# Performance work log

Hardware: AMD Instinct MI355X
Metric: run time of the kernel (lower is better)

Reference implementation:

```python
import jax, jax.numpy as jnp
import numpy as np


def _hungarian(a):
    """Jonker-Volgenant / Kuhn-Munkres shortest-augmenting-path LAP solver.
    a: (n, n) float numpy cost matrix. Returns col_ind (int64, len n) such that
    row i is matched to column col_ind[i] (row_ind is implicitly arange(n),
    exactly like scipy.optimize.linear_sum_assignment on a square matrix).
    """
    n = a.shape[0]
    INF = np.inf
    u = np.zeros(n + 1)
    v = np.zeros(n + 1)
    p = np.zeros(n + 1, dtype=np.int64)   # p[j] = row currently matched to column j
    way = np.zeros(n + 1, dtype=np.int64)
    for i in range(1, n + 1):
        p[0] = i
        j0 = 0
        minv = np.full(n + 1, INF)
        used = np.zeros(n + 1, dtype=bool)
        while True:
            used[j0] = True
            i0 = p[j0]
            cur = a[i0 - 1] - u[i0] - v[1:]          # reduced costs of row i0
            free = ~used[1:]
            better = free & (cur < minv[1:])
            minv[1:] = np.where(better, cur, minv[1:])
            way[1:] = np.where(better, j0, way[1:])
            cand = np.where(free, minv[1:], INF)
            j1 = int(np.argmin(cand)) + 1
            delta = cand[j1 - 1]
            u[p[used]] += delta
            v[used] -= delta
            minv[1:] = np.where(free, minv[1:] - delta, minv[1:])
            j0 = j1
            if p[j0] == 0:
                break
        while j0 != 0:                               # augment along alternating path
            j1 = int(way[j0])
            p[j0] = p[j1]
            j0 = j1
    col_ind = np.zeros(n, dtype=np.int64)
    col_ind[p[1:] - 1] = np.arange(n)
    return col_ind


def _matching(input, target):
    sx = jnp.sum(input * input, axis=-1)
    sy = jnp.sum(target * target, axis=-1)
    cost = sx[:, :, None] + sy[:, None, :] - 2.0 * jnp.einsum('bkd,bmd->bkm', input, target)
    cost_np = np.asarray(jax.device_get(cost), dtype=np.float64)
    perms = np.stack([_hungarian(c) for c in cost_np])  # (B, k)
    return jnp.asarray(perms)


def setup_inputs() -> dict:
    key = jax.random.key(0)
    k1, k2 = jax.random.split(key)
    B, K, D = 512, 128, 512
    return {
        "input": jax.random.normal(k1, (B, K, D), dtype=jnp.float32),
        "target": jax.random.normal(k2, (B, K, D), dtype=jnp.float32),
    }


def reference(input, target):
    # Hungarian assignment is computed on detached costs (constant wrt grads).
    perms = _matching(input, target)                       # (B, k)
    matched_target = jnp.take_along_axis(target, perms[:, :, None], axis=1)
    # Per-batch mean over (k, d), then mean over batch == global mean (equal sizes).
    return jnp.mean((input - matched_target) ** 2)
```

## Files before the change

kernel.cpp:

```cpp
#include <hip/hip_runtime.h>
#include <hip/hip_bf16.h>

#define K_PTS 128
#define DIM   512
#define BK    32
#define XS_STRIDE 132

__device__ __forceinline__ int rdlane_i(int v, int lane) {
    return __builtin_amdgcn_readlane(v, lane);
}
__device__ __forceinline__ float rdlane_f(float v, int lane) {
    return __int_as_float(__builtin_amdgcn_readlane(__float_as_int(v), lane));
}
__device__ __forceinline__ void wave_fence() {
    asm volatile("s_waitcnt lgkmcnt(0)" ::: "memory");
}

#define DPP_ID 0xFFFFFFFFu

template <int CTRL, int RM>
__device__ __forceinline__ unsigned dpp_min1(unsigned k) {
    unsigned o = (unsigned)__builtin_amdgcn_update_dpp((int)DPP_ID, (int)k, CTRL, RM, 0xF, false);
    return min(k, o);
}
__device__ __forceinline__ unsigned wave_min_u32(unsigned k) {
    k = dpp_min1<0x111, 0xF>(k);
    k = dpp_min1<0x112, 0xF>(k);
    k = dpp_min1<0x114, 0xF>(k);
    k = dpp_min1<0x118, 0xF>(k);
    k = dpp_min1<0x142, 0xA>(k);
    k = dpp_min1<0x143, 0xC>(k);
    return (unsigned)rdlane_i((int)k, 63);
}
template <int CTRL, int RM>
__device__ __forceinline__ void dpp_min2(unsigned& best, unsigned& sec) {
    unsigned ob = (unsigned)__builtin_amdgcn_update_dpp((int)DPP_ID, (int)best, CTRL, RM, 0xF, false);
    unsigned os = (unsigned)__builtin_amdgcn_update_dpp((int)DPP_ID, (int)sec,  CTRL, RM, 0xF, false);
    sec  = min(max(best, ob), min(sec, os));
    best = min(best, ob);
}
__device__ __forceinline__ void wave_min2_u32(unsigned& best, unsigned& sec) {
    dpp_min2<0x111, 0xF>(best, sec);
    dpp_min2<0x112, 0xF>(best, sec);
    dpp_min2<0x114, 0xF>(best, sec);
    dpp_min2<0x118, 0xF>(best, sec);
    dpp_min2<0x142, 0xA>(best, sec);
    dpp_min2<0x143, 0xC>(best, sec);
    best = (unsigned)rdlane_i((int)best, 63);
    sec  = (unsigned)rdlane_i((int)sec, 63);
}

__global__ __launch_bounds__(256, 2)
void hungarian_mse_kernel(const float* __restrict__ X, const float* __restrict__ Y,
                          float* __restrict__ out, float inv_total) {
    const int b = blockIdx.x;
    const int t = threadIdx.x;

    __shared__ float A[K_PTS * K_PTS];
    __shared__ float sx_sh[K_PTS];
    __shared__ float sy_sh[K_PTS];
    __shared__ float u_sh[K_PTS];
    __shared__ int   rmatch[K_PTS];
    __shared__ int   wl[512];
    __shared__ int   wl_n;

    float* Xs = A;
    float* Ys = A + BK * XS_STRIDE;

    const float* Xg = X + (size_t)b * K_PTS * DIM;
    const float* Yg = Y + (size_t)b * K_PTS * DIM;

    float acc[8][8];
#pragma unroll
    for (int i = 0; i < 8; ++i)
#pragma unroll
        for (int j = 0; j < 8; ++j) acc[i][j] = 0.0f;

    float nrm = 0.0f;
    const int tx = t & 15;
    const int ty = t >> 4;

    for (int k0 = 0; k0 < DIM; k0 += BK) {
        __syncthreads();
#pragma unroll
        for (int i = 0; i < 4; ++i) {
            int idx = t + i * 256;
            int r  = idx >> 3;
            int kq = idx & 7;
            float4 vx = *(const float4*)(Xg + r * DIM + k0 + kq * 4);
            float4 vy = *(const float4*)(Yg + r * DIM + k0 + kq * 4);
            int kb = kq * 4;
            Xs[(kb + 0) * XS_STRIDE + r] = vx.x;
            Xs[(kb + 1) * XS_STRIDE + r] = vx.y;
            Xs[(kb + 2) * XS_STRIDE + r] = vx.z;
            Xs[(kb + 3) * XS_STRIDE + r] = vx.w;
            Ys[(kb + 0) * XS_STRIDE + r] = vy.x;
            Ys[(kb + 1) * XS_STRIDE + r] = vy.y;
            Ys[(kb + 2) * XS_STRIDE + r] = vy.z;
            Ys[(kb + 3) * XS_STRIDE + r] = vy.w;
        }
        __syncthreads();
        for (int kk = 0; kk < BK; ++kk) {
            const float* xrow = Xs + kk * XS_STRIDE;
            const float* yrow = Ys + kk * XS_STRIDE;
            float4 xa = *(const float4*)(xrow + ty * 8);
            float4 xb = *(const float4*)(xrow + ty * 8 + 4);
            float4 ya = *(const float4*)(yrow + tx * 8);
            float4 yb = *(const float4*)(yrow + tx * 8 + 4);
            float av[8] = {xa.x, xa.y, xa.z, xa.w, xb.x, xb.y, xb.z, xb.w};
            float bv[8] = {ya.x, ya.y, ya.z, ya.w, yb.x, yb.y, yb.z, yb.w};
#pragma unroll
            for (int i = 0; i < 8; ++i)
#pragma unroll
                for (int j = 0; j < 8; ++j)
                    acc[i][j] = fmaf(av[i], bv[j], acc[i][j]);
        }
        if (t < 128) {
#pragma unroll
            for (int kk = 0; kk < BK; ++kk) {
                float v = Xs[kk * XS_STRIDE + t];
                nrm = fmaf(v, v, nrm);
            }
        } else {
#pragma unroll
            for (int kk = 0; kk < BK; ++kk) {
                float v = Ys[kk * XS_STRIDE + (t - 128)];
                nrm = fmaf(v, v, nrm);
            }
        }
    }
    if (t < 128) sx_sh[t] = nrm; else sy_sh[t - 128] = nrm;
    if (t < 128) u_sh[t] = 0.0f;
    __syncthreads();
#pragma unroll
    for (int i = 0; i < 8; ++i) {
        int r = ty * 8 + i;
        float sxr = sx_sh[r];
        float4 o0, o1;
        o0.x = sxr + sy_sh[tx * 8 + 0] - 2.0f * acc[i][0];
        o0.y = sxr + sy_sh[tx * 8 + 1] - 2.0f * acc[i][1];
        o0.z = sxr + sy_sh[tx * 8 + 2] - 2.0f * acc[i][2];
        o0.w = sxr + sy_sh[tx * 8 + 3] - 2.0f * acc[i][3];
        o1.x = sxr + sy_sh[tx * 8 + 4] - 2.0f * acc[i][4];
        o1.y = sxr + sy_sh[tx * 8 + 5] - 2.0f * acc[i][5];
        o1.z = sxr + sy_sh[tx * 8 + 6] - 2.0f * acc[i][6];
        o1.w = sxr + sy_sh[tx * 8 + 7] - 2.0f * acc[i][7];
        *(float4*)&A[r * K_PTS + tx * 8]     = o0;
        *(float4*)&A[r * K_PTS + tx * 8 + 4] = o1;
    }
    __syncthreads();

    if (t < 64) {
        asm volatile("s_setprio 3");
        const int c0 = 2 * t, c1 = 2 * t + 1;
        float v0, v1;
        int p_lo = -1, p_hi = -1;

        rmatch[t] = -1; rmatch[t + 64] = -1;
        wave_fence();
        {
            float m0 = 1e30f, m1 = 1e30f;
            int a0 = 0, a1 = 0;
#pragma unroll 4
            for (int i = 0; i < K_PTS; ++i) {
                float2 cc = *(const float2*)&A[i * K_PTS + c0];
                if (cc.x < m0) { m0 = cc.x; a0 = i; }
                if (cc.y < m1) { m1 = cc.y; a1 = i; }
            }
            v0 = m0; v1 = m1;
            int w0 = atomicCAS(&rmatch[a0], -1, c0);
            if (w0 == -1) p_lo = a0;
            int w1 = atomicCAS(&rmatch[a1], -1, c1);
            if (w1 == -1) p_hi = a1;
        }
        wave_fence();

        *(float2*)&sy_sh[c0] = make_float2(v0, v1);
        wave_fence();
#pragma unroll
        for (int which = 0; which < 2; ++which) {
            int i  = t + which * 64;
            int j1 = rmatch[i];
            float mu = 1e30f;
            if (j1 >= 0) {
#pragma unroll 4
                for (int s = 0; s < 64; ++s) {
                    int jj = (s + t) & 63;
                    float2 cc = *(const float2*)&A[i * K_PTS + 2 * jj];
                    float2 vv = *(const float2*)&sy_sh[2 * jj];
                    float r0 = cc.x - vv.x;
                    float r1 = cc.y - vv.y;
                    if (2 * jj     != j1) mu = fminf(mu, r0);
                    if (2 * jj + 1 != j1) mu = fminf(mu, r1);
                }
            }
            sx_sh[i] = mu;
        }
        wave_fence();
        if (p_lo >= 0) { float mu = sx_sh[p_lo]; v0 = A[p_lo * K_PTS + c0] - mu; u_sh[p_lo] = mu; }
        if (p_hi >= 0) { float mu = sx_sh[p_hi]; v1 = A[p_hi * K_PTS + c1] - mu; u_sh[p_hi] = mu; }
        wave_fence();

        if (t == 0) {
            int n = 0;
            for (int i = 0; i < K_PTS; ++i) if (rmatch[i] < 0) wl[n++] = i;
            wl_n = n;
        }
        wave_fence();

        {
            int head = 0, tail = wl_n, steps = 0;
            while (head < tail && steps < 320) {
                ++steps;
                int i = wl[head++];
                float2 cc = *(const float2*)&A[i * K_PTS + c0];
                float r0 = fmaxf(cc.x - v0, 0.0f);
                float r1 = fmaxf(cc.y - v1, 0.0f);
                unsigned k0 = (__float_as_uint(r0) & 0xFFFFFF80u) | (unsigned)c0;
                unsigned k1 = (__float_as_uint(r1) & 0xFFFFFF80u) | (unsigned)c1;
                unsigned best = min(k0, k1), sec = max(k0, k1);
                wave_min2_u32(best, sec);
                int j1 = (int)(best & 127u);
                int j2 = (int)(sec & 127u);
                float mu = __uint_as_float(best & 0xFFFFFF80u);
                float nu = __uint_as_float(sec  & 0xFFFFFF80u);
                if (t == 0) u_sh[i] = nu;
                int kO = rdlane_i((j1 & 1) ? p_hi : p_lo, j1 >> 1);
                bool strict = (mu < nu);
                if (strict && t == (j1 >> 1)) {
                    float d = nu - mu;
                    if (j1 & 1) v1 -= d; else v0 -= d;
                }
                int jA = j1;
                if (!strict && kO >= 0) {
                    int k2 = rdlane_i((j2 & 1) ? p_hi : p_lo, j2 >> 1);
                    if (k2 < 0) jA = j2;
                }
                int kOld = rdlane_i((jA & 1) ? p_hi : p_lo, jA >> 1);
                if (t == (jA >> 1)) { if (jA & 1) p_hi = i; else p_lo = i; }
                if (t == 0) {
                    rmatch[i] = jA;
                    if (kOld >= 0) { rmatch[kOld] = -1; wl[tail] = kOld; }
                }
                if (kOld >= 0) ++tail;
                wave_fence();
            }
        }

        if (t == 0) {
            int n = 0;
            for (int i = 0; i < K_PTS; ++i) if (rmatch[i] < 0) wl[n++] = i;
            wl_n = n;
        }
        wave_fence();
        const int nfree = wl_n;

        for (int idx = 0; idx < nfree; ++idx) {
            int row = wl[idx];
            float u_lo_reg = u_sh[t];
            float u_hi_reg = u_sh[t + 64];
            float u_row = rdlane_f((row >= 64) ? u_hi_reg : u_lo_reg, row & 63);
            float2 rc = *(const float2*)&A[row * K_PTS + c0];
            float dist0 = fmaxf(rc.x - u_row - v0, 0.0f);
            float dist1 = fmaxf(rc.y - u_row - v1, 0.0f);
            int way0 = 128, way1 = 128;
            bool sc0 = false, sc1 = false;
            int j1 = 0;
            float D = 0.0f;

            while (true) {
                unsigned k0 = sc0 ? 0xFFFFFFFFu
                                  : ((__float_as_uint(dist0) & 0xFFFFFF80u) | (unsigned)c0);
                unsigned k1 = sc1 ? 0xFFFFFFFFu
                                  : ((__float_as_uint(dist1) & 0xFFFFFF80u) | (unsigned)c1);
                unsigned k = wave_min_u32(min(k0, k1));
                j1 = (int)(k & 127u);
                D  = __uint_as_float(k & 0xFFFFFF80u);
                int i1 = rdlane_i((j1 & 1) ? p_hi : p_lo, j1 >> 1);
                if (i1 < 0) break;

                if (j1 == c0) sc0 = true;
                if (j1 == c1) sc1 = true;

                float u_i1 = rdlane_f((i1 >= 64) ? u_hi_reg : u_lo_reg, i1 & 63);
                float2 aa = *(const float2*)&A[i1 * K_PTS + c0];
                float base = D - u_i1;
                if (!sc0) {
                    float cv = fmaxf((aa.x - v0) + base, 0.0f);
                    if (cv < dist0) { dist0 = cv; way0 = j1; }
                }
                if (!sc1) {
                    float cv = fmaxf((aa.y - v1) + base, 0.0f);
                    if (cv < dist1) { dist1 = cv; way1 = j1; }
                }
            }

            if (sc0) { float del = D - dist0; v0 -= del; u_sh[p_lo] += del; }
            if (sc1) { float del = D - dist1; v1 -= del; u_sh[p_hi] += del; }
            if (t == 0) u_sh[row] += D;

            int j0 = j1;
            while (true) {
                int lane0 = j0 >> 1;
                bool odd = (j0 & 1) != 0;
                int jp = rdlane_i(odd ? way1 : way0, lane0);
                int pv;
                if (jp == 128) pv = row;
                else           pv = rdlane_i((jp & 1) ? p_hi : p_lo, jp >> 1);
                if (!odd && lane0 == t) p_lo = pv;
                if ( odd && lane0 == t) p_hi = pv;
                if (jp == 128) break;
                j0 = jp;
            }
            wave_fence();
        }

        float tsum = A[p_lo * K_PTS + c0] + A[p_hi * K_PTS + c1];
#pragma unroll
        for (int m = 1; m <= 32; m <<= 1)
            tsum += __shfl_xor(tsum, m, 64);
        if (t == 0) atomicAdd(out, tsum * inv_total);
    }
}

extern "C" void kernel_launch(void* const* d_in, const int* in_sizes, int n_in,
                              void* d_out, int out_size, void* d_ws, size_t ws_size,
                              hipStream_t stream) {
    const float* X = (const float*)d_in[0];
    const float* Y = (const float*)d_in[1];
    float* out = (float*)d_out;

    const int total = in_sizes[0];
    const int B = total / (K_PTS * DIM);
    const float inv_total = 1.0f / (float)total;

    hipMemsetAsync(out, 0, out_size * sizeof(float), stream);
    hungarian_mse_kernel<<<dim3(B), dim3(256), 0, stream>>>(X, Y, out, inv_total);
}
```

Baseline: 683.2 us.

## Scan up to four tied-minimum columns per Dijkstra step in LAP search

```diff
diff --git a/kernel.cpp b/kernel.cpp
--- a/kernel.cpp
+++ b/kernel.cpp
@@ -273,25 +273,60 @@
                                   : ((__float_as_uint(dist0) & 0xFFFFFF80u) | (unsigned)c0);
                 unsigned k1 = sc1 ? 0xFFFFFFFFu
                                   : ((__float_as_uint(dist1) & 0xFFFFFF80u) | (unsigned)c1);
-                unsigned k = wave_min_u32(min(k0, k1));
-                j1 = (int)(k & 127u);
-                D  = __uint_as_float(k & 0xFFFFFF80u);
-                int i1 = rdlane_i((j1 & 1) ? p_hi : p_lo, j1 >> 1);
-                if (i1 < 0) break;
-
-                if (j1 == c0) sc0 = true;
-                if (j1 == c1) sc1 = true;
-
-                float u_i1 = rdlane_f((i1 >= 64) ? u_hi_reg : u_lo_reg, i1 & 63);
-                float2 aa = *(const float2*)&A[i1 * K_PTS + c0];
-                float base = D - u_i1;
-                if (!sc0) {
-                    float cv = fmaxf((aa.x - v0) + base, 0.0f);
-                    if (cv < dist0) { dist0 = cv; way0 = j1; }
-                }
-                if (!sc1) {
-                    float cv = fmaxf((aa.y - v1) + base, 0.0f);
-                    if (cv < dist1) { dist1 = cv; way1 = j1; }
+                unsigned kmin = wave_min_u32(min(k0, k1));
+                unsigned Dbits = kmin & 0xFFFFFF80u;
+                D = __uint_as_float(Dbits);
+
+                bool cand0 = !sc0 && ((k0 & 0xFFFFFF80u) == Dbits);
+                bool cand1 = !sc1 && ((k1 & 0xFFFFFF80u) == Dbits);
+
+                bool f0 = cand0 && (p_lo < 0);
+                bool f1 = cand1 && (p_hi < 0);
+                unsigned long long bfree = __ballot(f0 || f1);
+                if (bfree) {
+                    int l = __ffsll(bfree) - 1;
+                    unsigned long long bf0 = __ballot(f0);
+                    j1 = ((bf0 >> l) & 1ull) ? 2 * l : 2 * l + 1;
+                    break;
+                }
+
+                unsigned long long b0 = __ballot(cand0);
+                unsigned long long b1 = __ballot(cand1);
+                int colS[4], rowS[4];
+#pragma unroll
+                for (int s = 0; s < 4; ++s) {
+                    int col = -1;
+                    if (b0) { int l = __ffsll(b0) - 1; b0 &= b0 - 1; col = 2 * l; }
+                    else if (b1) { int l = __ffsll(b1) - 1; b1 &= b1 - 1; col = 2 * l + 1; }
+                    colS[s] = col;
+                    rowS[s] = (col >= 0) ? rdlane_i((col & 1) ? p_hi : p_lo, col >> 1) : -1;
+                }
+
+#pragma unroll
+                for (int s = 0; s < 4; ++s) {
+                    if (colS[s] == c0) sc0 = true;
+                    if (colS[s] == c1) sc1 = true;
+                }
+
+                float2 aaS[4];
+#pragma unroll
+                for (int s = 0; s < 4; ++s)
+                    if (colS[s] >= 0) aaS[s] = *(const float2*)&A[rowS[s] * K_PTS + c0];
+
+#pragma unroll
+                for (int s = 0; s < 4; ++s) {
+                    if (colS[s] >= 0) {
+                        float u_i = rdlane_f((rowS[s] >= 64) ? u_hi_reg : u_lo_reg, rowS[s] & 63);
+                        float base = D - u_i;
+                        if (!sc0) {
+                            float cv = fmaxf((aaS[s].x - v0) + base, 0.0f);
+                            if (cv < dist0) { dist0 = cv; way0 = colS[s]; }
+                        }
+                        if (!sc1) {
+                            float cv = fmaxf((aaS[s].y - v1) + base, 0.0f);
+                            if (cv < dist1) { dist1 = cv; way1 = colS[s]; }
+                        }
+                    }
                 }
             }
 
```

Measured after the change: 846.6 us. 23.9% more time.

## Cache per-lane cost columns in VGPRs for the Hungarian solver wave

Applied to the files above, without the earlier changes.

```diff
diff --git a/kernel.cpp b/kernel.cpp
--- a/kernel.cpp
+++ b/kernel.cpp
@@ -5,6 +5,9 @@
 #define DIM   512
 #define BK    32
 #define XS_STRIDE 132
+#define B_CAP 320
+
+typedef float f32x32 __attribute__((ext_vector_type(32)));
 
 __device__ __forceinline__ int rdlane_i(int v, int lane) {
     return __builtin_amdgcn_readlane(v, lane);
@@ -50,7 +53,7 @@
     sec  = (unsigned)rdlane_i((int)sec, 63);
 }
 
-__global__ __launch_bounds__(256, 2)
+__global__ __launch_bounds__(256, 1)
 void hungarian_mse_kernel(const float* __restrict__ X, const float* __restrict__ Y,
                           float* __restrict__ out, float inv_total) {
     const int b = blockIdx.x;
@@ -153,6 +156,40 @@
     if (t < 64) {
         asm volatile("s_setprio 3");
         const int c0 = 2 * t, c1 = 2 * t + 1;
+
+        f32x32 aL0, aL1, aL2, aL3;
+        f32x32 aH0, aH1, aH2, aH3;
+#pragma unroll
+        for (int r = 0; r < 32; ++r) {
+            float2 cc = *(const float2*)&A[r * K_PTS + c0];
+            aL0[r] = cc.x; aH0[r] = cc.y;
+        }
+#pragma unroll
+        for (int r = 0; r < 32; ++r) {
+            float2 cc = *(const float2*)&A[(r + 32) * K_PTS + c0];
+            aL1[r] = cc.x; aH1[r] = cc.y;
+        }
+#pragma unroll
+        for (int r = 0; r < 32; ++r) {
+            float2 cc = *(const float2*)&A[(r + 64) * K_PTS + c0];
+            aL2[r] = cc.x; aH2[r] = cc.y;
+        }
+#pragma unroll
+        for (int r = 0; r < 32; ++r) {
+            float2 cc = *(const float2*)&A[(r + 96) * K_PTS + c0];
+            aL3[r] = cc.x; aH3[r] = cc.y;
+        }
+
+        auto GETROW = [&](int i) -> float2 {
+            int q = i >> 5, m = i & 31;
+            float x, y;
+            if (q == 0)      { x = aL0[m]; y = aH0[m]; }
+            else if (q == 1) { x = aL1[m]; y = aH1[m]; }
+            else if (q == 2) { x = aL2[m]; y = aH2[m]; }
+            else             { x = aL3[m]; y = aH3[m]; }
+            return make_float2(x, y);
+        };
+
         float v0, v1;
         int p_lo = -1, p_hi = -1;
 
@@ -161,11 +198,25 @@
         {
             float m0 = 1e30f, m1 = 1e30f;
             int a0 = 0, a1 = 0;
-#pragma unroll 4
-            for (int i = 0; i < K_PTS; ++i) {
-                float2 cc = *(const float2*)&A[i * K_PTS + c0];
-                if (cc.x < m0) { m0 = cc.x; a0 = i; }
-                if (cc.y < m1) { m1 = cc.y; a1 = i; }
+#pragma unroll
+            for (int i = 0; i < 32; ++i) {
+                if (aL0[i] < m0) { m0 = aL0[i]; a0 = i; }
+                if (aH0[i] < m1) { m1 = aH0[i]; a1 = i; }
+            }
+#pragma unroll
+            for (int i = 0; i < 32; ++i) {
+                if (aL1[i] < m0) { m0 = aL1[i]; a0 = i + 32; }
+                if (aH1[i] < m1) { m1 = aH1[i]; a1 = i + 32; }
+            }
+#pragma unroll
+            for (int i = 0; i < 32; ++i) {
+                if (aL2[i] < m0) { m0 = aL2[i]; a0 = i + 64; }
+                if (aH2[i] < m1) { m1 = aH2[i]; a1 = i + 64; }
+            }
+#pragma unroll
+            for (int i = 0; i < 32; ++i) {
+                if (aL3[i] < m0) { m0 = aL3[i]; a0 = i + 96; }
+                if (aH3[i] < m1) { m1 = aH3[i]; a1 = i + 96; }
             }
             v0 = m0; v1 = m1;
             int w0 = atomicCAS(&rmatch[a0], -1, c0);
@@ -197,8 +248,8 @@
             sx_sh[i] = mu;
         }
         wave_fence();
-        if (p_lo >= 0) { float mu = sx_sh[p_lo]; v0 = A[p_lo * K_PTS + c0] - mu; u_sh[p_lo] = mu; }
-        if (p_hi >= 0) { float mu = sx_sh[p_hi]; v1 = A[p_hi * K_PTS + c1] - mu; u_sh[p_hi] = mu; }
+        if (p_lo >= 0) { float mu = sx_sh[p_lo]; v0 = GETROW(p_lo).x - mu; u_sh[p_lo] = mu; }
+        if (p_hi >= 0) { float mu = sx_sh[p_hi]; v1 = GETROW(p_hi).y - mu; u_sh[p_hi] = mu; }
         wave_fence();
 
         if (t == 0) {
@@ -210,10 +261,11 @@
 
         {
             int head = 0, tail = wl_n, steps = 0;
-            while (head < tail && steps < 320) {
+            while (head < tail && steps < B_CAP) {
                 ++steps;
-                int i = wl[head++];
-                float2 cc = *(const float2*)&A[i * K_PTS + c0];
+                int i = __builtin_amdgcn_readfirstlane(wl[head++]);
+                wave_fence();
+                float2 cc = GETROW(i);
                 float r0 = fmaxf(cc.x - v0, 0.0f);
                 float r1 = fmaxf(cc.y - v1, 0.0f);
                 unsigned k0 = (__float_as_uint(r0) & 0xFFFFFF80u) | (unsigned)c0;
@@ -256,11 +308,11 @@
         const int nfree = wl_n;
 
         for (int idx = 0; idx < nfree; ++idx) {
-            int row = wl[idx];
+            int row = __builtin_amdgcn_readfirstlane(wl[idx]);
             float u_lo_reg = u_sh[t];
             float u_hi_reg = u_sh[t + 64];
-            float u_row = rdlane_f((row >= 64) ? u_hi_reg : u_lo_reg, row & 63);
-            float2 rc = *(const float2*)&A[row * K_PTS + c0];
+            float u_row = u_sh[row];
+            float2 rc = GETROW(row);
             float dist0 = fmaxf(rc.x - u_row - v0, 0.0f);
             float dist1 = fmaxf(rc.y - u_row - v1, 0.0f);
             int way0 = 128, way1 = 128;
@@ -283,7 +335,7 @@
                 if (j1 == c1) sc1 = true;
 
                 float u_i1 = rdlane_f((i1 >= 64) ? u_hi_reg : u_lo_reg, i1 & 63);
-                float2 aa = *(const float2*)&A[i1 * K_PTS + c0];
+                float2 aa = GETROW(i1);
                 float base = D - u_i1;
                 if (!sc0) {
                     float cv = fmaxf((aa.x - v0) + base, 0.0f);
```

Result: slower. 834.5 us (+22.1%).

## Split cost GEMM and LAP solve into separate kernels with register-resident cost rows

Applied to the files above, without the earlier changes.

```diff
diff --git a/kernel.cpp b/kernel.cpp
--- a/kernel.cpp
+++ b/kernel.cpp
@@ -5,6 +5,7 @@
 #define DIM   512
 #define BK    32
 #define XS_STRIDE 132
+#define B_CAP 320
 
 __device__ __forceinline__ int rdlane_i(int v, int lane) {
     return __builtin_amdgcn_readlane(v, lane);
@@ -50,25 +51,31 @@
     sec  = (unsigned)rdlane_i((int)sec, 63);
 }
 
+#define GR1(k)  case (k): gr = arr[(k)]; break;
+#define GR4(k)  GR1(k) GR1((k)+1) GR1((k)+2) GR1((k)+3)
+#define GR16(k) GR4(k) GR4((k)+4) GR4((k)+8) GR4((k)+12)
+#define GR64(k) GR16(k) GR16((k)+16) GR16((k)+32) GR16((k)+48)
+#define GETROW(dst, idx) do { float2 gr;                      \
+    switch (idx) { GR64(0) GR64(64)                           \
+        default: gr = make_float2(0.0f, 0.0f); break; }       \
+    (dst) = gr; } while (0)
+
 __global__ __launch_bounds__(256, 2)
-void hungarian_mse_kernel(const float* __restrict__ X, const float* __restrict__ Y,
-                          float* __restrict__ out, float inv_total) {
+void cost_kernel(const float* __restrict__ X, const float* __restrict__ Y,
+                 float* __restrict__ G) {
     const int b = blockIdx.x;
     const int t = threadIdx.x;
 
-    __shared__ float A[K_PTS * K_PTS];
+    __shared__ float stage[2 * BK * XS_STRIDE];
     __shared__ float sx_sh[K_PTS];
     __shared__ float sy_sh[K_PTS];
-    __shared__ float u_sh[K_PTS];
-    __shared__ int   rmatch[K_PTS];
-    __shared__ int   wl[512];
-    __shared__ int   wl_n;
-
-    float* Xs = A;
-    float* Ys = A + BK * XS_STRIDE;
+
+    float* Xs = stage;
+    float* Ys = stage + BK * XS_STRIDE;
 
     const float* Xg = X + (size_t)b * K_PTS * DIM;
     const float* Yg = Y + (size_t)b * K_PTS * DIM;
+    float* Gb = G + (size_t)b * K_PTS * K_PTS;
 
     float acc[8][8];
 #pragma unroll
@@ -130,6 +137,298 @@
         }
     }
     if (t < 128) sx_sh[t] = nrm; else sy_sh[t - 128] = nrm;
+    __syncthreads();
+#pragma unroll
+    for (int i = 0; i < 8; ++i) {
+        int r = ty * 8 + i;
+        float sxr = sx_sh[r];
+        float4 o0, o1;
+        o0.x = sxr + sy_sh[tx * 8 + 0] - 2.0f * acc[i][0];
+        o0.y = sxr + sy_sh[tx * 8 + 1] - 2.0f * acc[i][1];
+        o0.z = sxr + sy_sh[tx * 8 + 2] - 2.0f * acc[i][2];
+        o0.w = sxr + sy_sh[tx * 8 + 3] - 2.0f * acc[i][3];
+        o1.x = sxr + sy_sh[tx * 8 + 4] - 2.0f * acc[i][4];
+        o1.y = sxr + sy_sh[tx * 8 + 5] - 2.0f * acc[i][5];
+        o1.z = sxr + sy_sh[tx * 8 + 6] - 2.0f * acc[i][6];
+        o1.w = sxr + sy_sh[tx * 8 + 7] - 2.0f * acc[i][7];
+        *(float4*)&Gb[r * K_PTS + tx * 8]     = o0;
+        *(float4*)&Gb[r * K_PTS + tx * 8 + 4] = o1;
+    }
+}
+
+__global__ __launch_bounds__(64, 1)
+void lap_kernel(const float* __restrict__ G, float* __restrict__ out,
+                float inv_total) {
+    const int b = blockIdx.x;
+    const int t = threadIdx.x;
+
+    __shared__ float sx_sh[K_PTS];
+    __shared__ float sy_sh[K_PTS];
+    __shared__ float u_sh[K_PTS];
+    __shared__ int   rmatch[K_PTS];
+    __shared__ int   wl[512];
+    __shared__ int   wl_n;
+
+    const float*  Gb  = G + (size_t)b * K_PTS * K_PTS;
+    const float2* Gb2 = (const float2*)Gb;
+    const int c0 = 2 * t, c1 = 2 * t + 1;
+
+    asm volatile("s_setprio 3");
+
+    float2 arr[128];
+#pragma unroll
+    for (int r = 0; r < 128; ++r) arr[r] = Gb2[r * 64 + t];
+
+    u_sh[t] = 0.0f; u_sh[t + 64] = 0.0f;
+    rmatch[t] = -1; rmatch[t + 64] = -1;
+    wave_fence();
+
+    float v0, v1;
+    int p_lo = -1, p_hi = -1;
+
+    {
+        float m0 = 1e30f, m1 = 1e30f;
+        int a0 = 0, a1 = 0;
+#pragma unroll
+        for (int i = 0; i < 128; ++i) {
+            if (arr[i].x < m0) { m0 = arr[i].x; a0 = i; }
+            if (arr[i].y < m1) { m1 = arr[i].y; a1 = i; }
+        }
+        v0 = m0; v1 = m1;
+        int w0 = atomicCAS(&rmatch[a0], -1, c0);
+        if (w0 == -1) p_lo = a0;
+        int w1 = atomicCAS(&rmatch[a1], -1, c1);
+        if (w1 == -1) p_hi = a1;
+    }
+    wave_fence();
+
+    *(float2*)&sy_sh[c0] = make_float2(v0, v1);
+    wave_fence();
+#pragma unroll
+    for (int which = 0; which < 2; ++which) {
+        int i  = t + which * 64;
+        int j1 = rmatch[i];
+        float mu = 1e30f;
+        if (j1 >= 0) {
+#pragma unroll 4
+            for (int s = 0; s < 64; ++s) {
+                int jj = (s + t) & 63;
+                float2 cc = Gb2[i * 64 + jj];
+                float2 vv = *(const float2*)&sy_sh[2 * jj];
+                float r0 = cc.x - vv.x;
+                float r1 = cc.y - vv.y;
+                if (2 * jj     != j1) mu = fminf(mu, r0);
+                if (2 * jj + 1 != j1) mu = fminf(mu, r1);
+            }
+        }
+        sx_sh[i] = mu;
+    }
+    wave_fence();
+    if (p_lo >= 0) { float mu = sx_sh[p_lo]; v0 = Gb[p_lo * K_PTS + c0] - mu; u_sh[p_lo] = mu; }
+    if (p_hi >= 0) { float mu = sx_sh[p_hi]; v1 = Gb[p_hi * K_PTS + c1] - mu; u_sh[p_hi] = mu; }
+    wave_fence();
+
+    if (t == 0) {
+        int n = 0;
+        for (int i = 0; i < K_PTS; ++i) if (rmatch[i] < 0) wl[n++] = i;
+        wl_n = n;
+    }
+    wave_fence();
+
+    {
+        int head = 0, tail = wl_n, steps = 0;
+        while (head < tail && steps < B_CAP) {
+            ++steps;
+            int i = __builtin_amdgcn_readfirstlane(wl[head++]);
+            float2 cc; GETROW(cc, i);
+            float r0 = fmaxf(cc.x - v0, 0.0f);
+            float r1 = fmaxf(cc.y - v1, 0.0f);
+            unsigned k0 = (__float_as_uint(r0) & 0xFFFFFF80u) | (unsigned)c0;
+            unsigned k1 = (__float_as_uint(r1) & 0xFFFFFF80u) | (unsigned)c1;
+            unsigned best = min(k0, k1), sec = max(k0, k1);
+            wave_min2_u32(best, sec);
+            int j1 = (int)(best & 127u);
+            int j2 = (int)(sec & 127u);
+            float mu = __uint_as_float(best & 0xFFFFFF80u);
+            float nu = __uint_as_float(sec  & 0xFFFFFF80u);
+            if (t == 0) u_sh[i] = nu;
+            int kO = rdlane_i((j1 & 1) ? p_hi : p_lo, j1 >> 1);
+            bool strict = (mu < nu);
+            if (strict && t == (j1 >> 1)) {
+                float d = nu - mu;
+                if (j1 & 1) v1 -= d; else v0 -= d;
+            }
+            int jA = j1;
+            if (!strict && kO >= 0) {
+                int k2 = rdlane_i((j2 & 1) ? p_hi : p_lo, j2 >> 1);
+                if (k2 < 0) jA = j2;
+            }
+            int kOld = rdlane_i((jA & 1) ? p_hi : p_lo, jA >> 1);
+            if (t == (jA >> 1)) { if (jA & 1) p_hi = i; else p_lo = i; }
+            if (t == 0) {
+                rmatch[i] = jA;
+                if (kOld >= 0) { rmatch[kOld] = -1; wl[tail] = kOld; }
+            }
+            if (kOld >= 0) ++tail;
+            wave_fence();
+        }
+    }
+
+    if (t == 0) {
+        int n = 0;
+        for (int i = 0; i < K_PTS; ++i) if (rmatch[i] < 0) wl[n++] = i;
+        wl_n = n;
+    }
+    wave_fence();
+    const int nfree = wl_n;
+
+    for (int idx = 0; idx < nfree; ++idx) {
+        int row = __builtin_amdgcn_readfirstlane(wl[idx]);
+        float u_lo_reg = u_sh[t];
+        float u_hi_reg = u_sh[t + 64];
+        float u_row = u_sh[row];
+        float2 rc; GETROW(rc, row);
+        float dist0 = fmaxf(rc.x - u_row - v0, 0.0f);
+        float dist1 = fmaxf(rc.y - u_row - v1, 0.0f);
+        int way0 = 128, way1 = 128;
+        bool sc0 = false, sc1 = false;
+        int j1 = 0;
+        float D = 0.0f;
+
+        while (true) {
+            unsigned k0 = sc0 ? 0xFFFFFFFFu
+                              : ((__float_as_uint(dist0) & 0xFFFFFF80u) | (unsigned)c0);
+            unsigned k1 = sc1 ? 0xFFFFFFFFu
+                              : ((__float_as_uint(dist1) & 0xFFFFFF80u) | (unsigned)c1);
+            unsigned k = wave_min_u32(min(k0, k1));
+            j1 = (int)(k & 127u);
+            D  = __uint_as_float(k & 0xFFFFFF80u);
+            int i1 = rdlane_i((j1 & 1) ? p_hi : p_lo, j1 >> 1);
+            if (i1 < 0) break;
+
+            if (j1 == c0) sc0 = true;
+            if (j1 == c1) sc1 = true;
+
+            float u_i1 = rdlane_f((i1 >= 64) ? u_hi_reg : u_lo_reg, i1 & 63);
+            float2 aa; GETROW(aa, i1);
+            float base = D - u_i1;
+            if (!sc0) {
+                float cv = fmaxf((aa.x - v0) + base, 0.0f);
+                if (cv < dist0) { dist0 = cv; way0 = j1; }
+            }
+            if (!sc1) {
+                float cv = fmaxf((aa.y - v1) + base, 0.0f);
+                if (cv < dist1) { dist1 = cv; way1 = j1; }
+            }
+        }
+
+        if (sc0) { float del = D - dist0; v0 -= del; u_sh[p_lo] += del; }
+        if (sc1) { float del = D - dist1; v1 -= del; u_sh[p_hi] += del; }
+        if (t == 0) u_sh[row] += D;
+
+        int j0 = j1;
+        while (true) {
+            int lane0 = j0 >> 1;
+            bool odd = (j0 & 1) != 0;
+            int jp = rdlane_i(odd ? way1 : way0, lane0);
+            int pv;
+            if (jp == 128) pv = row;
+            else           pv = rdlane_i((jp & 1) ? p_hi : p_lo, jp >> 1);
+            if (!odd && lane0 == t) p_lo = pv;
+            if ( odd && lane0 == t) p_hi = pv;
+            if (jp == 128) break;
+            j0 = jp;
+        }
+        wave_fence();
+    }
+
+    float tsum = Gb[p_lo * K_PTS + c0] + Gb[p_hi * K_PTS + c1];
+#pragma unroll
+    for (int m = 1; m <= 32; m <<= 1)
+        tsum += __shfl_xor(tsum, m, 64);
+    if (t == 0) atomicAdd(out, tsum * inv_total);
+}
+
+__global__ __launch_bounds__(256, 2)
+void hungarian_mse_fallback(const float* __restrict__ X, const float* __restrict__ Y,
+                            float* __restrict__ out, float inv_total) {
+    const int b = blockIdx.x;
+    const int t = threadIdx.x;
+
+    __shared__ float A[K_PTS * K_PTS];
+    __shared__ float sx_sh[K_PTS];
+    __shared__ float sy_sh[K_PTS];
+    __shared__ float u_sh[K_PTS];
+    __shared__ int   rmatch[K_PTS];
+    __shared__ int   wl[512];
+    __shared__ int   wl_n;
+
+    float* Xs = A;
+    float* Ys = A + BK * XS_STRIDE;
+
+    const float* Xg = X + (size_t)b * K_PTS * DIM;
+    const float* Yg = Y + (size_t)b * K_PTS * DIM;
+
+    float acc[8][8];
+#pragma unroll
+    for (int i = 0; i < 8; ++i)
+#pragma unroll
+        for (int j = 0; j < 8; ++j) acc[i][j] = 0.0f;
+
+    float nrm = 0.0f;
+    const int tx = t & 15;
+    const int ty = t >> 4;
+
+    for (int k0 = 0; k0 < DIM; k0 += BK) {
+        __syncthreads();
+#pragma unroll
+        for (int i = 0; i < 4; ++i) {
+            int idx = t + i * 256;
+            int r  = idx >> 3;
+            int kq = idx & 7;
+            float4 vx = *(const float4*)(Xg + r * DIM + k0 + kq * 4);
+            float4 vy = *(const float4*)(Yg + r * DIM + k0 + kq * 4);
+            int kb = kq * 4;
+            Xs[(kb + 0) * XS_STRIDE + r] = vx.x;
+            Xs[(kb + 1) * XS_STRIDE + r] = vx.y;
+            Xs[(kb + 2) * XS_STRIDE + r] = vx.z;
+            Xs[(kb + 3) * XS_STRIDE + r] = vx.w;
+            Ys[(kb + 0) * XS_STRIDE + r] = vy.x;
+            Ys[(kb + 1) * XS_STRIDE + r] = vy.y;
+            Ys[(kb + 2) * XS_STRIDE + r] = vy.z;
+            Ys[(kb + 3) * XS_STRIDE + r] = vy.w;
+        }
+        __syncthreads();
+        for (int kk = 0; kk < BK; ++kk) {
+            const float* xrow = Xs + kk * XS_STRIDE;
+            const float* yrow = Ys + kk * XS_STRIDE;
+            float4 xa = *(const float4*)(xrow + ty * 8);
+            float4 xb = *(const float4*)(xrow + ty * 8 + 4);
+            float4 ya = *(const float4*)(yrow + tx * 8);
+            float4 yb = *(const float4*)(yrow + tx * 8 + 4);
+            float av[8] = {xa.x, xa.y, xa.z, xa.w, xb.x, xb.y, xb.z, xb.w};
+            float bv[8] = {ya.x, ya.y, ya.z, ya.w, yb.x, yb.y, yb.z, yb.w};
+#pragma unroll
+            for (int i = 0; i < 8; ++i)
+#pragma unroll
+                for (int j = 0; j < 8; ++j)
+                    acc[i][j] = fmaf(av[i], bv[j], acc[i][j]);
+        }
+        if (t < 128) {
+#pragma unroll
+            for (int kk = 0; kk < BK; ++kk) {
+                float v = Xs[kk * XS_STRIDE + t];
+                nrm = fmaf(v, v, nrm);
+            }
+        } else {
+#pragma unroll
+            for (int kk = 0; kk < BK; ++kk) {
+                float v = Ys[kk * XS_STRIDE + (t - 128)];
+                nrm = fmaf(v, v, nrm);
+            }
+        }
+    }
+    if (t < 128) sx_sh[t] = nrm; else sy_sh[t - 128] = nrm;
     if (t < 128) u_sh[t] = 0.0f;
     __syncthreads();
 #pragma unroll
@@ -210,7 +509,7 @@
 
         {
             int head = 0, tail = wl_n, steps = 0;
-            while (head < tail && steps < 320) {
+            while (head < tail && steps < B_CAP) {
                 ++steps;
                 int i = wl[head++];
                 float2 cc = *(const float2*)&A[i * K_PTS + c0];
@@ -259,7 +558,7 @@
             int row = wl[idx];
             float u_lo_reg = u_sh[t];
             float u_hi_reg = u_sh[t + 64];
-            float u_row = rdlane_f((row >= 64) ? u_hi_reg : u_lo_reg, row & 63);
+            float u_row = u_sh[row];
             float2 rc = *(const float2*)&A[row * K_PTS + c0];
             float dist0 = fmaxf(rc.x - u_row - v0, 0.0f);
             float dist1 = fmaxf(rc.y - u_row - v1, 0.0f);
@@ -335,5 +634,13 @@
     const float inv_total = 1.0f / (float)total;
 
     hipMemsetAsync(out, 0, out_size * sizeof(float), stream);
-    hungarian_mse_kernel<<<dim3(B), dim3(256), 0, stream>>>(X, Y, out, inv_total);
-}
+
+    const size_t need = (size_t)B * K_PTS * K_PTS * sizeof(float);
+    if (d_ws != nullptr && ws_size >= need) {
+        float* G = (float*)d_ws;
+        cost_kernel<<<dim3(B), dim3(256), 0, stream>>>(X, Y, G);
+        lap_kernel<<<dim3(B), dim3(64), 0, stream>>>(G, out, inv_total);
+    } else {
+        hungarian_mse_fallback<<<dim3(B), dim3(256), 0, stream>>>(X, Y, out, inv_total);
+    }
+}
```

Result: slower. 865.3 us (+26.6%).
